# Performance work log

Measured on AMD Instinct MI355X. Metric: run time of the kernel, lower is better.

The kernel has to match this reference:

```python
import jax, jax.numpy as jnp
import numpy as np

N = 4096      # nodes
FIN = 512     # input features
HID = 256     # hidden_features (concat across heads)
H = 4         # n_heads in layer 1
D1 = HID // H # per-head dim layer 1
C = 64        # num_classes
NEG = 0.2     # leaky_relu slope


def setup_inputs() -> dict:
    key = jax.random.key(0)
    ks = jax.random.split(key, 8)
    x = jax.random.normal(ks[0], (N, FIN), jnp.float32)
    A = jax.random.randint(ks[1], (N, N), 0, 2, jnp.int32)
    A = jnp.maximum(A, jnp.eye(N, dtype=jnp.int32))  # self-loops: no all-masked rows
    s = 0.05
    W1 = jax.random.normal(ks[2], (FIN, H * D1), jnp.float32) * s
    a1_src = jax.random.normal(ks[3], (H, D1), jnp.float32) * s
    a1_dst = jax.random.normal(ks[4], (H, D1), jnp.float32) * s
    W2 = jax.random.normal(ks[5], (HID, C), jnp.float32) * s
    a2_src = jax.random.normal(ks[6], (1, C), jnp.float32) * s
    a2_dst = jax.random.normal(ks[7], (1, C), jnp.float32) * s
    return {"x": x, "A": A, "W1": W1, "a1_src": a1_src, "a1_dst": a1_dst,
            "W2": W2, "a2_src": a2_src, "a2_dst": a2_dst}


def gat_layer(x, A, W, a_src, a_dst, is_concat):
    n = x.shape[0]
    h_heads, d = a_src.shape
    h = (x @ W).reshape(n, h_heads, d)                 # [N,H,D]
    s_src = jnp.einsum('nhd,hd->nh', h, a_src)          # [N,H]
    s_dst = jnp.einsum('nhd,hd->nh', h, a_dst)          # [N,H]
    e = s_src[:, None, :] + s_dst[None, :, :]           # [N,N,H]
    e = jnp.where(e >= 0, e, NEG * e)                   # LeakyReLU
    mask = (A > 0)[:, :, None]
    e = jnp.where(mask, e, jnp.float32(-1e9))           # adjacency mask
    alpha = jax.nn.softmax(e, axis=1)                   # softmax over neighbors j
    out = jnp.einsum('ijh,jhd->ihd', alpha, h)          # aggregate
    return out.reshape(n, h_heads * d) if is_concat else out.mean(axis=1)


def reference(x, A, W1, a1_src, a1_dst, W2, a2_src, a2_dst):
    h = gat_layer(x, A, W1, a1_src, a1_dst, True)
    h = jax.nn.elu(h)
    return gat_layer(h, A, W2, a2_src, a2_dst, False)
```

## Files before the change

kernel.cpp:

```cpp
#include <hip/hip_runtime.h>
#include <hip/hip_bf16.h>

#define NN 4096
#define FIN 512
#define HID 256
#define NH 4
#define DD 64
#define NCLS 64

typedef short bf16x8 __attribute__((ext_vector_type(8)));
typedef float f32x4 __attribute__((ext_vector_type(4)));
typedef unsigned int u32x4 __attribute__((ext_vector_type(4)));

__device__ __forceinline__ unsigned fbits(float x) {
    return __builtin_bit_cast(unsigned, x);
}
__device__ __forceinline__ unsigned short f2bf_rne(float x) {
    unsigned u = fbits(x);
    unsigned r = (u + 0x7fffu + ((u >> 16) & 1u)) >> 16;
    return (unsigned short)r;
}

__device__ __forceinline__ bf16x8 pack8(const float* wv) {
    u32x4 au;
#pragma unroll
    for (int t = 0; t < 4; ++t)
        au[t] = (fbits(wv[2 * t]) >> 16) | (fbits(wv[2 * t + 1]) & 0xffff0000u);
    return __builtin_bit_cast(bf16x8, au);
}

__device__ __forceinline__ bf16x8 ones_frag() {
    u32x4 au = {0x3f803f80u, 0x3f803f80u, 0x3f803f80u, 0x3f803f80u};
    return __builtin_bit_cast(bf16x8, au);
}

__device__ __forceinline__ void compute_probe(int m, int quad, int* pi, int* pn) {
    float xv[8], yv[8];
#pragma unroll
    for (int e = 0; e < 8; ++e) {
        xv[e] = (quad == 0 && e == 0) ? (float)(m + 1) : 0.f;
        yv[e] = (quad == 0 && e == 0) ? 1.f : 0.f;
    }
    bf16x8 x1 = pack8(xv), y1 = pack8(yv);
#pragma unroll
    for (int e = 0; e < 8; ++e) {
        xv[e] = (quad == 0 && e == 0) ? 1.f : 0.f;
        yv[e] = (quad == 0 && e == 0) ? (float)(m + 1) : 0.f;
    }
    bf16x8 x2 = pack8(xv), y2 = pack8(yv);
    f32x4 d1 = {}, d2 = {};
    d1 = __builtin_amdgcn_mfma_f32_16x16x32_bf16(x1, y1, d1, 0, 0, 0);
    d2 = __builtin_amdgcn_mfma_f32_16x16x32_bf16(x2, y2, d2, 0, 0, 0);
#pragma unroll
    for (int r = 0; r < 4; ++r) {
        pi[r] = min(15, max(0, (int)d1[r] - 1));
        pn[r] = min(15, max(0, (int)d2[r] - 1));
    }
}

__global__ __launch_bounds__(256) void adj_bitmask(const int* __restrict__ Adj,
                                                   unsigned* __restrict__ Adjb) {
    const size_t base = (size_t)blockIdx.x * 1024;
    const int tid = threadIdx.x, lane = tid & 63;
#pragma unroll
    for (int c = 0; c < 4; ++c) {
        size_t gid = base + c * 256 + tid;
        int v = Adj[gid];
        unsigned long long bm = __ballot(v > 0);
        if ((lane & 31) == 0)
            Adjb[gid >> 5] = (unsigned)((lane & 32) ? (bm >> 32) : bm);
    }
}

template <int R, int C>
__global__ __launch_bounds__(256) void transpose_cvt(const float* __restrict__ In,
                                                     unsigned short* __restrict__ OutT) {
    __shared__ float t[32][33];
    const int tid = threadIdx.x;
    const int r0 = blockIdx.y * 32, c0 = blockIdx.x * 32;
    const int rl = tid >> 3, cg = tid & 7;
    float4 v = *(const float4*)&In[(size_t)(r0 + rl) * C + c0 + cg * 4];
    t[rl][cg * 4 + 0] = v.x; t[rl][cg * 4 + 1] = v.y;
    t[rl][cg * 4 + 2] = v.z; t[rl][cg * 4 + 3] = v.w;
    __syncthreads();
    const int cl = tid >> 3, rg = tid & 7;
    ushort4 o;
    o.x = f2bf_rne(t[rg * 4 + 0][cl]);
    o.y = f2bf_rne(t[rg * 4 + 1][cl]);
    o.z = f2bf_rne(t[rg * 4 + 2][cl]);
    o.w = f2bf_rne(t[rg * 4 + 3][cl]);
    *(ushort4*)&OutT[(size_t)(c0 + cl) * R + r0 + rg * 4] = o;
}

template <int K, bool ABF>
__global__ __launch_bounds__(256) void gemm_head(
    const void* __restrict__ Ap,
    const unsigned short* __restrict__ WT,
    const float* __restrict__ a_src, const float* __restrict__ a_dst,
    unsigned short* __restrict__ HT,
    float* __restrict__ ssr,
    float* __restrict__ EP)
{
    __shared__ float accx[4][16][65];
    __shared__ unsigned short hbf[16][64];
    const int tid = threadIdx.x;
    const int lane = tid & 63, sp = tid >> 6;
    const int m = lane & 15, quad = lane >> 4;
    const int hh = blockIdx.x, i0 = blockIdx.y * 16;
    const int n0 = hh * 64;
    int pi[4], pn[4];
    compute_probe(m, quad, pi, pn);
    f32x4 acc[4] = {};
    constexpr int KS = K / 128;

    bf16x8 a[2], b[2][4];
    auto load_a = [&](int ks) -> bf16x8 {
        const int kb = sp * (K / 4) + ks * 32 + quad * 8;
        if (ABF) {
            return *(const bf16x8*)((const unsigned short*)Ap + (size_t)(i0 + m) * K + kb);
        } else {
            const float* Af = (const float*)Ap + (size_t)(i0 + m) * K + kb;
            float4 a0 = *(const float4*)Af;
            float4 a1 = *(const float4*)(Af + 4);
            float av8[8] = {a0.x, a0.y, a0.z, a0.w, a1.x, a1.y, a1.z, a1.w};
            u32x4 au;
#pragma unroll
            for (int t = 0; t < 4; ++t) {
                unsigned lo = (unsigned)f2bf_rne(av8[2 * t]);
                unsigned hi = (unsigned)f2bf_rne(av8[2 * t + 1]) << 16;
                au[t] = lo | hi;
            }
            return __builtin_bit_cast(bf16x8, au);
        }
    };
    a[0] = load_a(0);
#pragma unroll
    for (int nt = 0; nt < 4; ++nt) {
        const int kb = sp * (K / 4) + quad * 8;
        b[0][nt] = *(const bf16x8*)&WT[(size_t)(n0 + nt * 16 + m) * K + kb];
    }
#pragma unroll
    for (int ks = 0; ks < KS; ++ks) {
        const int cur = ks & 1, nxt = cur ^ 1;
        if (ks + 1 < KS) {
            a[nxt] = load_a(ks + 1);
            const int kb = sp * (K / 4) + (ks + 1) * 32 + quad * 8;
#pragma unroll
            for (int nt = 0; nt < 4; ++nt)
                b[nxt][nt] = *(const bf16x8*)&WT[(size_t)(n0 + nt * 16 + m) * K + kb];
        }
#pragma unroll
        for (int nt = 0; nt < 4; ++nt)
            acc[nt] = __builtin_amdgcn_mfma_f32_16x16x32_bf16(a[cur], b[cur][nt], acc[nt], 0, 0, 0);
    }
#pragma unroll
    for (int nt = 0; nt < 4; ++nt)
#pragma unroll
        for (int r = 0; r < 4; ++r)
            accx[sp][pi[r]][nt * 16 + pn[r]] = acc[nt][r];
    __syncthreads();

    const int row = tid >> 4, cg = tid & 15;
    float ps = 0.f, pd = 0.f;
#pragma unroll
    for (int c4 = 0; c4 < 4; ++c4) {
        int col = cg * 4 + c4;
        float val = accx[0][row][col] + accx[1][row][col] +
                    accx[2][row][col] + accx[3][row][col];
        ps += val * a_src[n0 + col];
        pd += val * a_dst[n0 + col];
        hbf[row][col] = f2bf_rne(val);
    }
#pragma unroll
    for (int o = 8; o >= 1; o >>= 1) {
        ps += __shfl_xor(ps, o, 64);
        pd += __shfl_xor(pd, o, 64);
    }
    if (cg == 0) {
        int node = i0 + row;
        ssr[hh * NN + node] = ps;
        EP[(size_t)(hh * NN + node) * 2 + 0] = __expf(pd);
        EP[(size_t)(hh * NN + node) * 2 + 1] = __expf(0.2f * pd);
    }
    __syncthreads();
    const int c = tid >> 2, rq = tid & 3;
    ushort4 o4;
    o4.x = hbf[rq * 4 + 0][c];
    o4.y = hbf[rq * 4 + 1][c];
    o4.z = hbf[rq * 4 + 2][c];
    o4.w = hbf[rq * 4 + 3][c];
    *(ushort4*)&HT[(size_t)(n0 + c) * NN + i0 + rq * 4] = o4;
}

template <int IT, int NSTEP>
__device__ __forceinline__ void attn_core_mt(
    const unsigned short* __restrict__ htb,
    const unsigned* __restrict__ Adjb,
    const float* __restrict__ ssh,
    const float* __restrict__ eph,
    const int i0, const int jbase, const int m, const int quad,
    f32x4 (&acc)[IT][4], f32x4 (&accd)[IT])
{
    const bf16x8 ones = ones_frag();
    const unsigned* mrow[IT];
    float E1i[IT], E2i[IT];
#pragma unroll
    for (int t = 0; t < IT; ++t) {
        float ss = ssh[i0 + t * 16 + m];
        E1i[t] = __expf(ss);
        E2i[t] = __expf(0.2f * ss);
        mrow[t] = Adjb + (size_t)(i0 + t * 16 + m) * 128 + (jbase >> 5);
    }
    u32x4 mwb[2][IT];
    f32x4 ep[2][4];
    bf16x8 bf[2][4];
#pragma unroll
    for (int t = 0; t < IT; ++t) mwb[0][t] = *(const u32x4*)mrow[t];
    {
        const int kb = jbase + quad * 8;
        const float* e = eph + 2 * kb;
#pragma unroll
        for (int v = 0; v < 4; ++v) ep[0][v] = *(const f32x4*)(e + 4 * v);
#pragma unroll
        for (int nt = 0; nt < 4; ++nt)
            bf[0][nt] = *(const bf16x8*)&htb[(size_t)(nt * 16 + m) * NN + kb];
    }
#pragma unroll
    for (int s = 0; s < NSTEP; ++s) {
        const int cur = s & 1, nxt = cur ^ 1;
        if (s + 1 < NSTEP) {
            const int kb = jbase + (s + 1) * 32 + quad * 8;
            const float* e = eph + 2 * kb;
#pragma unroll
            for (int v = 0; v < 4; ++v) ep[nxt][v] = *(const f32x4*)(e + 4 * v);
#pragma unroll
            for (int nt = 0; nt < 4; ++nt)
                bf[nxt][nt] = *(const bf16x8*)&htb[(size_t)(nt * 16 + m) * NN + kb];
        }
        if ((s & 3) == 0 && s + 4 < NSTEP) {
#pragma unroll
            for (int t = 0; t < IT; ++t)
                mwb[((s >> 2) + 1) & 1][t] =
                    *(const u32x4*)(mrow[t] + (s >> 2) * 4 + 4);
        }
#pragma unroll
        for (int t = 0; t < IT; ++t) {
            const unsigned mb = (mwb[(s >> 2) & 1][t][s & 3] >> (quad * 8)) & 0xffu;
            float wv[8];
#pragma unroll
            for (int u = 0; u < 8; ++u) {
                float e1 = ep[cur][u >> 1][(2 * u) & 3];
                float e2 = ep[cur][u >> 1][(2 * u + 1) & 3];
                float w = fmaxf(E1i[t] * e1, E2i[t] * e2);
                wv[u] = ((mb >> u) & 1u) ? w : 0.f;
            }
            bf16x8 av = pack8(wv);
            accd[t] = __builtin_amdgcn_mfma_f32_16x16x32_bf16(av, ones, accd[t], 0, 0, 0);
#pragma unroll
            for (int nt = 0; nt < 4; ++nt)
                acc[t][nt] = __builtin_amdgcn_mfma_f32_16x16x32_bf16(
                    av, bf[cur][nt], acc[t][nt], 0, 0, 0);
        }
    }
}

__global__ __launch_bounds__(512, 2) void attn_l1(
    const unsigned short* __restrict__ HT,
    const unsigned* __restrict__ Adjb,
    const float* __restrict__ ssr,
    const float* __restrict__ EP,
    unsigned short* __restrict__ Outb)
{
    __shared__ float accx[4][8][16][65];
    __shared__ float lx[4][8][16];
    const int tid = threadIdx.x;
    const int lane = tid & 63, sp = tid >> 6;
    const int m = lane & 15, quad = lane >> 4;
    const int i0 = blockIdx.x * 64, hh = blockIdx.y;
    int pi[4], pn[4];
    compute_probe(m, quad, pi, pn);

    const unsigned short* htb = HT + (size_t)(hh * 64) * NN;
    const float* eph = EP + (size_t)hh * NN * 2;
    const float* ssh = ssr + hh * NN;

    f32x4 acc[4][4] = {};
    f32x4 accd[4] = {};
    attn_core_mt<4, 16>(htb, Adjb, ssh, eph, i0, sp * 512, m, quad, acc, accd);

#pragma unroll
    for (int t = 0; t < 4; ++t) {
#pragma unroll
        for (int nt = 0; nt < 4; ++nt)
#pragma unroll
            for (int r = 0; r < 4; ++r)
                accx[t][sp][pi[r]][nt * 16 + pn[r]] = acc[t][nt][r];
#pragma unroll
        for (int r = 0; r < 4; ++r) lx[t][sp][pi[r]] = accd[t][r];
    }
    __syncthreads();

#pragma unroll
    for (int e = 0; e < 8; ++e) {
        int idx = tid + e * 512;
        int t = idx >> 10, row = (idx >> 6) & 15, col = idx & 63;
        float num = 0.f, den = 0.f;
#pragma unroll
        for (int s = 0; s < 8; ++s) {
            num += accx[t][s][row][col];
            den += lx[t][s][row];
        }
        float o = num / den;
        o = (o > 0.f) ? o : (__expf(o) - 1.f);
        Outb[(size_t)(i0 + t * 16 + row) * HID + hh * 64 + col] = f2bf_rne(o);
    }
}

__global__ __launch_bounds__(512, 2) void attn_l2(
    const unsigned short* __restrict__ HT,
    const unsigned* __restrict__ Adjb,
    const float* __restrict__ ssr,
    const float* __restrict__ EP,
    float* __restrict__ Out)
{
    __shared__ float accx[8][16][65];
    __shared__ float lx[8][16];
    const int tid = threadIdx.x;
    const int lane = tid & 63, sp = tid >> 6;
    const int m = lane & 15, quad = lane >> 4;
    const int i0 = blockIdx.x * 16;
    int pi[4], pn[4];
    compute_probe(m, quad, pi, pn);

    f32x4 acc[1][4] = {};
    f32x4 accd[1] = {};
    attn_core_mt<1, 16>(HT, Adjb, ssr, EP, i0, sp * 512, m, quad, acc, accd);

#pragma unroll
    for (int nt = 0; nt < 4; ++nt)
#pragma unroll
        for (int r = 0; r < 4; ++r)
            accx[sp][pi[r]][nt * 16 + pn[r]] = acc[0][nt][r];
#pragma unroll
    for (int r = 0; r < 4; ++r) lx[sp][pi[r]] = accd[0][r];
    __syncthreads();

#pragma unroll
    for (int e = 0; e < 2; ++e) {
        int idx = tid + e * 512;
        int row = idx >> 6, col = idx & 63;
        float num = 0.f, den = 0.f;
#pragma unroll
        for (int s = 0; s < 8; ++s) {
            num += accx[s][row][col];
            den += lx[s][row];
        }
        Out[(size_t)(i0 + row) * NCLS + col] = num / den;
    }
}

extern "C" void kernel_launch(void* const* d_in, const int* in_sizes, int n_in,
                              void* d_out, int out_size, void* d_ws, size_t ws_size,
                              hipStream_t stream) {
    const float* x      = (const float*)d_in[0];
    const int*   Adj    = (const int*)d_in[1];
    const float* W1     = (const float*)d_in[2];
    const float* a1_src = (const float*)d_in[3];
    const float* a1_dst = (const float*)d_in[4];
    const float* W2     = (const float*)d_in[5];
    const float* a2_src = (const float*)d_in[6];
    const float* a2_dst = (const float*)d_in[7];
    float* out = (float*)d_out;

    float* ws = (float*)d_ws;
    unsigned short* HT1  = (unsigned short*)ws;
    unsigned short* HT2  = (unsigned short*)(ws + 524288);
    unsigned short* h1e  = (unsigned short*)(ws + 655360);
    unsigned short* WT1  = (unsigned short*)(ws + 1179648);
    unsigned short* WT2  = (unsigned short*)(ws + 1245184);
    unsigned*       Adjb = (unsigned*)(ws + 1253376);
    float* s1s = ws + 1777664;
    float* EP1 = ws + 1794048;
    float* s2s = ws + 1826816;
    float* EP2 = ws + 1830912;

    adj_bitmask<<<dim3(16384), 256, 0, stream>>>(Adj, Adjb);
    transpose_cvt<FIN, HID><<<dim3(HID / 32, FIN / 32), 256, 0, stream>>>(W1, WT1);
    transpose_cvt<HID, NCLS><<<dim3(NCLS / 32, HID / 32), 256, 0, stream>>>(W2, WT2);

    gemm_head<FIN, false><<<dim3(NH, NN / 16), 256, 0, stream>>>(
        x, WT1, a1_src, a1_dst, HT1, s1s, EP1);
    attn_l1<<<dim3(NN / 64, NH), 512, 0, stream>>>(HT1, Adjb, s1s, EP1, h1e);

    gemm_head<HID, true><<<dim3(1, NN / 16), 256, 0, stream>>>(
        h1e, WT2, a2_src, a2_dst, HT2, s2s, EP2);
    attn_l2<<<dim3(NN / 16), 512, 0, stream>>>(HT2, Adjb, s2s, EP2, out);
}
```

Baseline: 190.9 us.

## Split attention neighbor range across blocks and fuse combine into next GEMM

The attention kernels now split the neighbor dimension into two halves across a new grid axis and write partial numerators and denominators to workspace. Layer-1 normalization and ELU are folded into the layer-2 projection GEMM, and a small combine kernel finishes layer 2. Per-block tile size drops (32 rows, 256 columns per wave) and occupancy hints rise to 4 blocks per CU, with double-buffered prefetch replaced by simple loops. This aims to raise parallelism and occupancy, at the cost of extra fp32 partial-sum traffic and one more launch.

```diff
diff --git a/kernel.cpp b/kernel.cpp
--- a/kernel.cpp
+++ b/kernel.cpp
@@ -25,7 +25,8 @@
     u32x4 au;
 #pragma unroll
     for (int t = 0; t < 4; ++t)
-        au[t] = (fbits(wv[2 * t]) >> 16) | (fbits(wv[2 * t + 1]) & 0xffff0000u);
+        au[t] = __builtin_amdgcn_perm(fbits(wv[2 * t + 1]), fbits(wv[2 * t]),
+                                      0x07060302u);
     return __builtin_bit_cast(bf16x8, au);
 }
 
@@ -92,14 +93,50 @@
     *(ushort4*)&OutT[(size_t)(c0 + cl) * R + r0 + rg * 4] = o;
 }
 
-template <int K, bool ABF>
-__global__ __launch_bounds__(256) void gemm_head(
-    const void* __restrict__ Ap,
+__device__ __forceinline__ void head_epilogue(
+    float (*accx)[16][65], unsigned short (*hbf)[64],
+    int tid, int hh, int i0, int n0,
+    const float* a_src, const float* a_dst,
+    unsigned short* HT, float* ssr, float* EP)
+{
+    const int row = tid >> 4, cg = tid & 15;
+    float ps = 0.f, pd = 0.f;
+#pragma unroll
+    for (int c4 = 0; c4 < 4; ++c4) {
+        int col = cg * 4 + c4;
+        float val = accx[0][row][col] + accx[1][row][col] +
+                    accx[2][row][col] + accx[3][row][col];
+        ps += val * a_src[n0 + col];
+        pd += val * a_dst[n0 + col];
+        hbf[row][col] = f2bf_rne(val);
+    }
+#pragma unroll
+    for (int o = 8; o >= 1; o >>= 1) {
+        ps += __shfl_xor(ps, o, 64);
+        pd += __shfl_xor(pd, o, 64);
+    }
+    if (cg == 0) {
+        int node = i0 + row;
+        ssr[hh * NN + node] = ps;
+        EP[(size_t)(hh * NN + node) * 2 + 0] = __expf(pd);
+        EP[(size_t)(hh * NN + node) * 2 + 1] = __expf(0.2f * pd);
+    }
+    __syncthreads();
+    const int c = tid >> 2, rq = tid & 3;
+    ushort4 o4;
+    o4.x = hbf[rq * 4 + 0][c];
+    o4.y = hbf[rq * 4 + 1][c];
+    o4.z = hbf[rq * 4 + 2][c];
+    o4.w = hbf[rq * 4 + 3][c];
+    *(ushort4*)&HT[(size_t)(n0 + c) * NN + i0 + rq * 4] = o4;
+}
+
+__global__ __launch_bounds__(256) void gemm_head1(
+    const float* __restrict__ x,
     const unsigned short* __restrict__ WT,
     const float* __restrict__ a_src, const float* __restrict__ a_dst,
     unsigned short* __restrict__ HT,
-    float* __restrict__ ssr,
-    float* __restrict__ EP)
+    float* __restrict__ ssr, float* __restrict__ EP)
 {
     __shared__ float accx[4][16][65];
     __shared__ unsigned short hbf[16][64];
@@ -111,47 +148,26 @@
     int pi[4], pn[4];
     compute_probe(m, quad, pi, pn);
     f32x4 acc[4] = {};
-    constexpr int KS = K / 128;
-
-    bf16x8 a[2], b[2][4];
-    auto load_a = [&](int ks) -> bf16x8 {
-        const int kb = sp * (K / 4) + ks * 32 + quad * 8;
-        if (ABF) {
-            return *(const bf16x8*)((const unsigned short*)Ap + (size_t)(i0 + m) * K + kb);
-        } else {
-            const float* Af = (const float*)Ap + (size_t)(i0 + m) * K + kb;
-            float4 a0 = *(const float4*)Af;
-            float4 a1 = *(const float4*)(Af + 4);
-            float av8[8] = {a0.x, a0.y, a0.z, a0.w, a1.x, a1.y, a1.z, a1.w};
-            u32x4 au;
-#pragma unroll
-            for (int t = 0; t < 4; ++t) {
-                unsigned lo = (unsigned)f2bf_rne(av8[2 * t]);
-                unsigned hi = (unsigned)f2bf_rne(av8[2 * t + 1]) << 16;
-                au[t] = lo | hi;
-            }
-            return __builtin_bit_cast(bf16x8, au);
-        }
-    };
-    a[0] = load_a(0);
-#pragma unroll
-    for (int nt = 0; nt < 4; ++nt) {
-        const int kb = sp * (K / 4) + quad * 8;
-        b[0][nt] = *(const bf16x8*)&WT[(size_t)(n0 + nt * 16 + m) * K + kb];
-    }
-#pragma unroll
-    for (int ks = 0; ks < KS; ++ks) {
-        const int cur = ks & 1, nxt = cur ^ 1;
-        if (ks + 1 < KS) {
-            a[nxt] = load_a(ks + 1);
-            const int kb = sp * (K / 4) + (ks + 1) * 32 + quad * 8;
-#pragma unroll
-            for (int nt = 0; nt < 4; ++nt)
-                b[nxt][nt] = *(const bf16x8*)&WT[(size_t)(n0 + nt * 16 + m) * K + kb];
-        }
-#pragma unroll
-        for (int nt = 0; nt < 4; ++nt)
-            acc[nt] = __builtin_amdgcn_mfma_f32_16x16x32_bf16(a[cur], b[cur][nt], acc[nt], 0, 0, 0);
+#pragma unroll
+    for (int ks = 0; ks < 4; ++ks) {
+        const int kb = sp * 128 + ks * 32 + quad * 8;
+        const float* Af = x + (size_t)(i0 + m) * FIN + kb;
+        float4 a0 = *(const float4*)Af;
+        float4 a1 = *(const float4*)(Af + 4);
+        float av8[8] = {a0.x, a0.y, a0.z, a0.w, a1.x, a1.y, a1.z, a1.w};
+        u32x4 au;
+#pragma unroll
+        for (int t = 0; t < 4; ++t)
+            au[t] = (unsigned)f2bf_rne(av8[2 * t]) |
+                    ((unsigned)f2bf_rne(av8[2 * t + 1]) << 16);
+        bf16x8 a = __builtin_bit_cast(bf16x8, au);
+        bf16x8 b[4];
+#pragma unroll
+        for (int nt = 0; nt < 4; ++nt)
+            b[nt] = *(const bf16x8*)&WT[(size_t)(n0 + nt * 16 + m) * FIN + kb];
+#pragma unroll
+        for (int nt = 0; nt < 4; ++nt)
+            acc[nt] = __builtin_amdgcn_mfma_f32_16x16x32_bf16(a, b[nt], acc[nt], 0, 0, 0);
     }
 #pragma unroll
     for (int nt = 0; nt < 4; ++nt)
@@ -159,41 +175,69 @@
         for (int r = 0; r < 4; ++r)
             accx[sp][pi[r]][nt * 16 + pn[r]] = acc[nt][r];
     __syncthreads();
-
-    const int row = tid >> 4, cg = tid & 15;
-    float ps = 0.f, pd = 0.f;
-#pragma unroll
-    for (int c4 = 0; c4 < 4; ++c4) {
-        int col = cg * 4 + c4;
-        float val = accx[0][row][col] + accx[1][row][col] +
-                    accx[2][row][col] + accx[3][row][col];
-        ps += val * a_src[n0 + col];
-        pd += val * a_dst[n0 + col];
-        hbf[row][col] = f2bf_rne(val);
-    }
-#pragma unroll
-    for (int o = 8; o >= 1; o >>= 1) {
-        ps += __shfl_xor(ps, o, 64);
-        pd += __shfl_xor(pd, o, 64);
-    }
-    if (cg == 0) {
-        int node = i0 + row;
-        ssr[hh * NN + node] = ps;
-        EP[(size_t)(hh * NN + node) * 2 + 0] = __expf(pd);
-        EP[(size_t)(hh * NN + node) * 2 + 1] = __expf(0.2f * pd);
-    }
-    __syncthreads();
-    const int c = tid >> 2, rq = tid & 3;
-    ushort4 o4;
-    o4.x = hbf[rq * 4 + 0][c];
-    o4.y = hbf[rq * 4 + 1][c];
-    o4.z = hbf[rq * 4 + 2][c];
-    o4.w = hbf[rq * 4 + 3][c];
-    *(ushort4*)&HT[(size_t)(n0 + c) * NN + i0 + rq * 4] = o4;
-}
-
-template <int IT, int NSTEP>
-__device__ __forceinline__ void attn_core_mt(
+    head_epilogue(accx, hbf, tid, hh, i0, n0, a_src, a_dst, HT, ssr, EP);
+}
+
+__global__ __launch_bounds__(256) void gemm_head2(
+    const float* __restrict__ numP,
+    const float* __restrict__ denP,
+    const unsigned short* __restrict__ WT,
+    const float* __restrict__ a_src, const float* __restrict__ a_dst,
+    unsigned short* __restrict__ HT,
+    float* __restrict__ ssr, float* __restrict__ EP)
+{
+    __shared__ float accx[4][16][65];
+    __shared__ unsigned short hbf[16][64];
+    const int tid = threadIdx.x;
+    const int lane = tid & 63, sp = tid >> 6;
+    const int m = lane & 15, quad = lane >> 4;
+    const int i0 = blockIdx.x * 16;
+    int pi[4], pn[4];
+    compute_probe(m, quad, pi, pn);
+
+    const float rd = 1.f / (denP[sp * NN + i0 + m] +
+                            denP[NH * NN + sp * NN + i0 + m]);
+    f32x4 acc[4] = {};
+#pragma unroll
+    for (int ks = 0; ks < 2; ++ks) {
+        const int kb = sp * 64 + ks * 32 + quad * 8;
+        const float* p0 = numP + (size_t)(i0 + m) * HID + kb;
+        const float* p1 = p0 + (size_t)NN * HID;
+        float4 a0 = *(const float4*)p0;
+        float4 a1 = *(const float4*)(p0 + 4);
+        float4 b0 = *(const float4*)p1;
+        float4 b1 = *(const float4*)(p1 + 4);
+        float av8[8] = {a0.x + b0.x, a0.y + b0.y, a0.z + b0.z, a0.w + b0.w,
+                        a1.x + b1.x, a1.y + b1.y, a1.z + b1.z, a1.w + b1.w};
+        u32x4 au;
+#pragma unroll
+        for (int t = 0; t < 4; ++t) {
+            float v0 = av8[2 * t] * rd;
+            float v1 = av8[2 * t + 1] * rd;
+            v0 = (v0 > 0.f) ? v0 : (__expf(v0) - 1.f);
+            v1 = (v1 > 0.f) ? v1 : (__expf(v1) - 1.f);
+            au[t] = (unsigned)f2bf_rne(v0) | ((unsigned)f2bf_rne(v1) << 16);
+        }
+        bf16x8 a = __builtin_bit_cast(bf16x8, au);
+        bf16x8 b[4];
+#pragma unroll
+        for (int nt = 0; nt < 4; ++nt)
+            b[nt] = *(const bf16x8*)&WT[(size_t)(nt * 16 + m) * HID + kb];
+#pragma unroll
+        for (int nt = 0; nt < 4; ++nt)
+            acc[nt] = __builtin_amdgcn_mfma_f32_16x16x32_bf16(a, b[nt], acc[nt], 0, 0, 0);
+    }
+#pragma unroll
+    for (int nt = 0; nt < 4; ++nt)
+#pragma unroll
+        for (int r = 0; r < 4; ++r)
+            accx[sp][pi[r]][nt * 16 + pn[r]] = acc[nt][r];
+    __syncthreads();
+    head_epilogue(accx, hbf, tid, 0, i0, 0, a_src, a_dst, HT, ssr, EP);
+}
+
+template <int IT>
+__device__ __forceinline__ void attn_core2(
     const unsigned short* __restrict__ htb,
     const unsigned* __restrict__ Adjb,
     const float* __restrict__ ssh,
@@ -202,55 +246,36 @@
     f32x4 (&acc)[IT][4], f32x4 (&accd)[IT])
 {
     const bf16x8 ones = ones_frag();
-    const unsigned* mrow[IT];
     float E1i[IT], E2i[IT];
+    u32x4 mw[IT][2];
 #pragma unroll
     for (int t = 0; t < IT; ++t) {
         float ss = ssh[i0 + t * 16 + m];
         E1i[t] = __expf(ss);
         E2i[t] = __expf(0.2f * ss);
-        mrow[t] = Adjb + (size_t)(i0 + t * 16 + m) * 128 + (jbase >> 5);
-    }
-    u32x4 mwb[2][IT];
-    f32x4 ep[2][4];
-    bf16x8 bf[2][4];
-#pragma unroll
-    for (int t = 0; t < IT; ++t) mwb[0][t] = *(const u32x4*)mrow[t];
-    {
-        const int kb = jbase + quad * 8;
+        const unsigned* mrow = Adjb + (size_t)(i0 + t * 16 + m) * 128 + (jbase >> 5);
+        mw[t][0] = *(const u32x4*)mrow;
+        mw[t][1] = *(const u32x4*)(mrow + 4);
+    }
+#pragma unroll
+    for (int s = 0; s < 8; ++s) {
+        const int kb = jbase + s * 32 + quad * 8;
         const float* e = eph + 2 * kb;
-#pragma unroll
-        for (int v = 0; v < 4; ++v) ep[0][v] = *(const f32x4*)(e + 4 * v);
-#pragma unroll
-        for (int nt = 0; nt < 4; ++nt)
-            bf[0][nt] = *(const bf16x8*)&htb[(size_t)(nt * 16 + m) * NN + kb];
-    }
-#pragma unroll
-    for (int s = 0; s < NSTEP; ++s) {
-        const int cur = s & 1, nxt = cur ^ 1;
-        if (s + 1 < NSTEP) {
-            const int kb = jbase + (s + 1) * 32 + quad * 8;
-            const float* e = eph + 2 * kb;
-#pragma unroll
-            for (int v = 0; v < 4; ++v) ep[nxt][v] = *(const f32x4*)(e + 4 * v);
-#pragma unroll
-            for (int nt = 0; nt < 4; ++nt)
-                bf[nxt][nt] = *(const bf16x8*)&htb[(size_t)(nt * 16 + m) * NN + kb];
-        }
-        if ((s & 3) == 0 && s + 4 < NSTEP) {
-#pragma unroll
-            for (int t = 0; t < IT; ++t)
-                mwb[((s >> 2) + 1) & 1][t] =
-                    *(const u32x4*)(mrow[t] + (s >> 2) * 4 + 4);
-        }
+        f32x4 ep[4];
+#pragma unroll
+        for (int v = 0; v < 4; ++v) ep[v] = *(const f32x4*)(e + 4 * v);
+        bf16x8 bf[4];
+#pragma unroll
+        for (int nt = 0; nt < 4; ++nt)
+            bf[nt] = *(const bf16x8*)&htb[(size_t)(nt * 16 + m) * NN + kb];
 #pragma unroll
         for (int t = 0; t < IT; ++t) {
-            const unsigned mb = (mwb[(s >> 2) & 1][t][s & 3] >> (quad * 8)) & 0xffu;
+            const unsigned mb = (mw[t][s >> 2][s & 3] >> (quad * 8)) & 0xffu;
             float wv[8];
 #pragma unroll
             for (int u = 0; u < 8; ++u) {
-                float e1 = ep[cur][u >> 1][(2 * u) & 3];
-                float e2 = ep[cur][u >> 1][(2 * u + 1) & 3];
+                float e1 = ep[u >> 1][(2 * u) & 3];
+                float e2 = ep[u >> 1][(2 * u + 1) & 3];
                 float w = fmaxf(E1i[t] * e1, E2i[t] * e2);
                 wv[u] = ((mb >> u) & 1u) ? w : 0.f;
             }
@@ -259,37 +284,39 @@
 #pragma unroll
             for (int nt = 0; nt < 4; ++nt)
                 acc[t][nt] = __builtin_amdgcn_mfma_f32_16x16x32_bf16(
-                    av, bf[cur][nt], acc[t][nt], 0, 0, 0);
+                    av, bf[nt], acc[t][nt], 0, 0, 0);
         }
     }
 }
 
-__global__ __launch_bounds__(512, 2) void attn_l1(
+__global__ __launch_bounds__(512, 4) void attn_l1(
     const unsigned short* __restrict__ HT,
     const unsigned* __restrict__ Adjb,
     const float* __restrict__ ssr,
     const float* __restrict__ EP,
-    unsigned short* __restrict__ Outb)
-{
-    __shared__ float accx[4][8][16][65];
-    __shared__ float lx[4][8][16];
+    float* __restrict__ numP,
+    float* __restrict__ denP)
+{
+    __shared__ float accx[2][8][16][65];
+    __shared__ float lx[2][8][16];
     const int tid = threadIdx.x;
     const int lane = tid & 63, sp = tid >> 6;
     const int m = lane & 15, quad = lane >> 4;
-    const int i0 = blockIdx.x * 64, hh = blockIdx.y;
+    const int i0 = blockIdx.x * 32, hh = blockIdx.y, half = blockIdx.z;
     int pi[4], pn[4];
     compute_probe(m, quad, pi, pn);
 
     const unsigned short* htb = HT + (size_t)(hh * 64) * NN;
     const float* eph = EP + (size_t)hh * NN * 2;
     const float* ssh = ssr + hh * NN;
-
-    f32x4 acc[4][4] = {};
-    f32x4 accd[4] = {};
-    attn_core_mt<4, 16>(htb, Adjb, ssh, eph, i0, sp * 512, m, quad, acc, accd);
-
-#pragma unroll
-    for (int t = 0; t < 4; ++t) {
+    const int jbase = half * 2048 + sp * 256;
+
+    f32x4 acc[2][4] = {};
+    f32x4 accd[2] = {};
+    attn_core2<2>(htb, Adjb, ssh, eph, i0, jbase, m, quad, acc, accd);
+
+#pragma unroll
+    for (int t = 0; t < 2; ++t) {
 #pragma unroll
         for (int nt = 0; nt < 4; ++nt)
 #pragma unroll
@@ -301,7 +328,7 @@
     __syncthreads();
 
 #pragma unroll
-    for (int e = 0; e < 8; ++e) {
+    for (int e = 0; e < 4; ++e) {
         int idx = tid + e * 512;
         int t = idx >> 10, row = (idx >> 6) & 15, col = idx & 63;
         float num = 0.f, den = 0.f;
@@ -310,31 +337,33 @@
             num += accx[t][s][row][col];
             den += lx[t][s][row];
         }
-        float o = num / den;
-        o = (o > 0.f) ? o : (__expf(o) - 1.f);
-        Outb[(size_t)(i0 + t * 16 + row) * HID + hh * 64 + col] = f2bf_rne(o);
-    }
-}
-
-__global__ __launch_bounds__(512, 2) void attn_l2(
+        int node = i0 + t * 16 + row;
+        numP[(size_t)half * NN * HID + (size_t)node * HID + hh * 64 + col] = num;
+        if (col == 0) denP[(size_t)half * NH * NN + hh * NN + node] = den;
+    }
+}
+
+__global__ __launch_bounds__(512, 4) void attn_l2(
     const unsigned short* __restrict__ HT,
     const unsigned* __restrict__ Adjb,
     const float* __restrict__ ssr,
     const float* __restrict__ EP,
-    float* __restrict__ Out)
+    float* __restrict__ numP,
+    float* __restrict__ denP)
 {
     __shared__ float accx[8][16][65];
     __shared__ float lx[8][16];
     const int tid = threadIdx.x;
     const int lane = tid & 63, sp = tid >> 6;
     const int m = lane & 15, quad = lane >> 4;
-    const int i0 = blockIdx.x * 16;
+    const int i0 = blockIdx.x * 16, half = blockIdx.y;
     int pi[4], pn[4];
     compute_probe(m, quad, pi, pn);
+    const int jbase = half * 2048 + sp * 256;
 
     f32x4 acc[1][4] = {};
     f32x4 accd[1] = {};
-    attn_core_mt<1, 16>(HT, Adjb, ssr, EP, i0, sp * 512, m, quad, acc, accd);
+    attn_core2<1>(HT, Adjb, ssr, EP, i0, jbase, m, quad, acc, accd);
 
 #pragma unroll
     for (int nt = 0; nt < 4; ++nt)
@@ -355,8 +384,25 @@
             num += accx[s][row][col];
             den += lx[s][row];
         }
-        Out[(size_t)(i0 + row) * NCLS + col] = num / den;
-    }
+        int node = i0 + row;
+        numP[(size_t)half * NN * 64 + (size_t)node * 64 + col] = num;
+        if (col == 0) denP[(size_t)half * NN + node] = den;
+    }
+}
+
+__global__ __launch_bounds__(256) void combine_out(
+    const float* __restrict__ numP, const float* __restrict__ denP,
+    float* __restrict__ out)
+{
+    const int gid = blockIdx.x * 256 + threadIdx.x;
+    const int base = gid * 4;
+    const int node = base >> 6;
+    float4 n0 = *(const float4*)&numP[base];
+    float4 n1 = *(const float4*)&numP[(size_t)NN * 64 + base];
+    float rd = 1.f / (denP[node] + denP[NN + node]);
+    float4 o = make_float4((n0.x + n1.x) * rd, (n0.y + n1.y) * rd,
+                           (n0.z + n1.z) * rd, (n0.w + n1.w) * rd);
+    *(float4*)&out[base] = o;
 }
 
 extern "C" void kernel_launch(void* const* d_in, const int* in_sizes, int n_in,
@@ -373,26 +419,32 @@
     float* out = (float*)d_out;
 
     float* ws = (float*)d_ws;
-    unsigned short* HT1  = (unsigned short*)ws;
-    unsigned short* HT2  = (unsigned short*)(ws + 524288);
-    unsigned short* h1e  = (unsigned short*)(ws + 655360);
-    unsigned short* WT1  = (unsigned short*)(ws + 1179648);
-    unsigned short* WT2  = (unsigned short*)(ws + 1245184);
-    unsigned*       Adjb = (unsigned*)(ws + 1253376);
-    float* s1s = ws + 1777664;
-    float* EP1 = ws + 1794048;
-    float* s2s = ws + 1826816;
-    float* EP2 = ws + 1830912;
+    unsigned short* HT1   = (unsigned short*)ws;
+    float*          numP1 = ws + 524288;
+    float*          denP1 = ws + 2621440;
+    unsigned short* HT2   = (unsigned short*)(ws + 2654208);
+    unsigned short* WT1   = (unsigned short*)(ws + 2785280);
+    unsigned short* WT2   = (unsigned short*)(ws + 2850816);
+    unsigned*       Adjb  = (unsigned*)(ws + 2859008);
+    float* s1s   = ws + 3383296;
+    float* EP1   = ws + 3399680;
+    float* s2s   = ws + 3432448;
+    float* EP2   = ws + 3436544;
+    float* numP2 = ws + 3444736;
+    float* denP2 = ws + 3969024;
 
     adj_bitmask<<<dim3(16384), 256, 0, stream>>>(Adj, Adjb);
     transpose_cvt<FIN, HID><<<dim3(HID / 32, FIN / 32), 256, 0, stream>>>(W1, WT1);
     transpose_cvt<HID, NCLS><<<dim3(NCLS / 32, HID / 32), 256, 0, stream>>>(W2, WT2);
 
-    gemm_head<FIN, false><<<dim3(NH, NN / 16), 256, 0, stream>>>(
+    gemm_head1<<<dim3(NH, NN / 16), 256, 0, stream>>>(
         x, WT1, a1_src, a1_dst, HT1, s1s, EP1);
-    attn_l1<<<dim3(NN / 64, NH), 512, 0, stream>>>(HT1, Adjb, s1s, EP1, h1e);
-
-    gemm_head<HID, true><<<dim3(1, NN / 16), 256, 0, stream>>>(
-        h1e, WT2, a2_src, a2_dst, HT2, s2s, EP2);
-    attn_l2<<<dim3(NN / 16), 512, 0, stream>>>(HT2, Adjb, s2s, EP2, out);
-}
+    attn_l1<<<dim3(NN / 32, NH, 2), 512, 0, stream>>>(
+        HT1, Adjb, s1s, EP1, numP1, denP1);
+
+    gemm_head2<<<dim3(NN / 16), 256, 0, stream>>>(
+        numP1, denP1, WT2, a2_src, a2_dst, HT2, s2s, EP2);
+    attn_l2<<<dim3(NN / 16, 2), 512, 0, stream>>>(
+        HT2, Adjb, s2s, EP2, numP2, denP2);
+    combine_out<<<dim3(256), 256, 0, stream>>>(numP2, denP2, out);
+}
```

Result: slower. 206.6 us (+8.2%).
